# Kernel tuning notes

Measured on AMD Instinct MI355X. Metric: run time of the kernel, lower is better.

The kernel has to match this reference:

```python
import jax, jax.numpy as jnp
import numpy as np

B, L, D, K = 16, 1024, 1024, 3
EPS_LN = 1e-5    # nn.LayerNorm default eps inside SRUCell
EPS_RMS = 1e-6   # RMSNorm eps
HIGHWAY_BIAS = -2.0


def setup_inputs() -> dict:
    key = jax.random.key(0)
    ks = jax.random.split(key, 8)
    x = jax.random.normal(ks[0], (B, L, D), jnp.float32)
    conv_w = jax.random.normal(ks[1], (D, D, K), jnp.float32) * (1.0 / np.sqrt(D * K))
    conv_b = jax.random.normal(ks[2], (D,), jnp.float32) * 0.01
    ln_g = jnp.ones((D,), jnp.float32)
    ln_b = jnp.zeros((D,), jnp.float32)
    sru_w = jax.random.normal(ks[3], (D, 3 * D), jnp.float32) * (1.0 / np.sqrt(D))
    sru_v = jax.random.uniform(ks[4], (2 * D,), jnp.float32, -0.18, 0.18)
    # SRU init: forget-gate bias 0, reset-gate bias = highway_bias
    sru_b = jnp.concatenate([jnp.zeros((D,), jnp.float32),
                             jnp.full((D,), HIGHWAY_BIAS, jnp.float32)])
    lambda_w = jax.random.normal(ks[5], (D,), jnp.float32)
    rms_w = jnp.ones((D,), jnp.float32)
    return {"x": x, "conv_w": conv_w, "conv_b": conv_b, "ln_g": ln_g,
            "ln_b": ln_b, "sru_w": sru_w, "sru_v": sru_v, "sru_b": sru_b,
            "lambda_w": lambda_w, "rms_w": rms_w}


def reference(x, conv_w, conv_b, ln_g, ln_b, sru_w, sru_v, sru_b, lambda_w, rms_w):
    # --- causal conv1d: left-pad K-1 zeros, 'VALID' conv -> same length ---
    xT = jnp.transpose(x, (0, 2, 1))                      # (B, D, L)
    xp = jnp.pad(xT, ((0, 0), (0, 0), (K - 1, 0)))
    y = jax.lax.conv_general_dilated(
        xp, conv_w, window_strides=(1,), padding='VALID',
        dimension_numbers=('NCH', 'OIH', 'NCH')) + conv_b[None, :, None]
    cnn_out = jnp.transpose(y, (2, 0, 1))                 # (L, B, D) time-major

    # --- SRUCell with layer_norm=True: LN on input, then U = x @ W (k=3) ---
    mu = jnp.mean(cnn_out, -1, keepdims=True)
    var = jnp.mean((cnn_out - mu) ** 2, -1, keepdims=True)
    normed = (cnn_out - mu) * jax.lax.rsqrt(var + EPS_LN) * ln_g + ln_b
    U = jnp.einsum('lbd,de->lbe', normed, sru_w).reshape(L, B, D, 3)

    v_f, v_r = sru_v[:D], sru_v[D:]
    b_f, b_r = sru_b[:D], sru_b[D:]

    def step(c, inputs):
        u, xt = inputs                                    # u: (B, D, 3), xt: (B, D)
        u0, u1, u2 = u[..., 0], u[..., 1], u[..., 2]
        f = jax.nn.sigmoid(u1 + v_f * c + b_f)
        c_new = f * c + (1.0 - f) * u0
        r = jax.nn.sigmoid(u2 + v_r * c + b_r)
        h = r * jnp.tanh(c_new) + (1.0 - r) * xt          # highway (scale_x = 1)
        return c_new, h

    c0 = jnp.zeros((B, D), jnp.float32)
    _, h = jax.lax.scan(step, c0, (U, normed))            # h: (L, B, D)

    # --- lambda-weighted residual mix ---
    out = lambda_w * cnn_out + (1.0 - lambda_w) * h       # (L, B, D)
    out = jnp.transpose(out, (1, 0, 2))                   # (B, L, D)

    # --- RMSNorm (dropout is identity in eval) ---
    rms = out * jax.lax.rsqrt(jnp.mean(out * out, -1, keepdims=True) + EPS_RMS)
    return rms_w * rms
```

## Files before the change

### kernel.cpp

```cpp
#include <hip/hip_runtime.h>
#include <cstdint>
#include <cstddef>

#define LL 1024
#define DD 1024
#define BB 16

typedef _Float16 f16;
typedef _Float16 f16x8 __attribute__((ext_vector_type(8)));
typedef _Float16 f16x4 __attribute__((ext_vector_type(4)));
typedef float f32x4 __attribute__((ext_vector_type(4)));

__global__ __launch_bounds__(256) void xsplit_kernel(const float* __restrict__ x,
                                                     f16* __restrict__ xh) {
    int i = blockIdx.x * 256 + threadIdx.x;
    const int total = BB * LL * DD / 4;
    if (i >= total) return;
    float4 v = ((const float4*)x)[i];
    f16x4 h;
    h[0] = (f16)v.x; h[1] = (f16)v.y; h[2] = (f16)v.z; h[3] = (f16)v.w;
    ((f16x4*)xh)[i] = h;
}

__global__ __launch_bounds__(256) void wkt_kernel(const float* __restrict__ w,
                                                  f16* __restrict__ wkT) {
    int idx = blockIdx.x * 256 + threadIdx.x;
    if (idx >= 3 * DD * DD) return;
    int o = idx / 3072;
    int r = idx - o * 3072;
    int k = r >> 10, i = r & 1023;
    wkT[idx] = (f16)w[(size_t)o * 3072 + i * 3 + k];
}

__global__ __launch_bounds__(256) void swt_kernel(const float* __restrict__ w,
                                                  f16* __restrict__ swT) {
    int idx = blockIdx.x * 256 + threadIdx.x;
    if (idx >= 3 * DD * DD) return;
    int e = idx >> 10, d = idx & 1023;
    swT[idx] = (f16)w[(size_t)d * 3072 + e];
}

__global__ __launch_bounds__(256) void hgemm_kernel(
    const f16* __restrict__ A, const f16* __restrict__ BT,
    const float* __restrict__ bias, float* __restrict__ C,
    int N, int Kdim, int mode, int l0, int tpb, int Lc) {
    __shared__ f16 Asm[128 * 64];
    __shared__ f16 Bsm[128 * 64];
    const int tid = threadIdx.x;
    const int lane = tid & 63, wave = tid >> 6;
    const int wm = wave & 1, wn = wave >> 1;
    const int n0 = blockIdx.x * 128;

    int arowbase, crowbase;
    if (mode == 0) {
        arowbase = blockIdx.y * 128;
        crowbase = arowbase;
    } else {
        int bb = blockIdx.y / tpb, lt = blockIdx.y - bb * tpb;
        arowbase = (bb << 10) + l0 + lt * 128;
        crowbase = bb * Lc + lt * 128;
    }

    const int srow = tid >> 1;
    const int scb = (tid & 1) * 4;

    auto loadA = [&](int kt, f16x8 (&pa)[4]) {
#pragma unroll
        for (int q = 0; q < 4; ++q) {
            int sc = scb + q;
            if (mode == 0) {
                int m = arowbase + srow;
                int bb2 = m >> 10, l = m & 1023;
                int kc = kt >> 10;
                int t = l + kc - 2;
                int i0 = (kt & 1023) + sc * 8;
                if (t < 0) {
                    f16x8 z;
#pragma unroll
                    for (int e = 0; e < 8; ++e) z[e] = (f16)0;
                    pa[q] = z;
                } else {
                    pa[q] = *(const f16x8*)(A + (((size_t)(bb2 << 10) + t) << 10) + i0);
                }
            } else {
                pa[q] = *(const f16x8*)(A + ((size_t)(arowbase + srow) << 10) + kt + sc * 8);
            }
        }
    };
    auto loadB = [&](int kt, f16x8 (&pb)[4]) {
#pragma unroll
        for (int q = 0; q < 4; ++q) {
            int sc = scb + q;
            pb[q] = *(const f16x8*)(BT + (size_t)(n0 + srow) * Kdim + kt + sc * 8);
        }
    };
    auto store_sm = [&](f16* sm, f16x8 (&p)[4]) {
#pragma unroll
        for (int q = 0; q < 4; ++q) {
            int sc = scb + q;
            int byte = srow * 128 + ((sc * 16) ^ ((srow & 7) << 4));
            *(f16x8*)((char*)sm + byte) = p[q];
        }
    };

    f32x4 acc[4][4];
#pragma unroll
    for (int i = 0; i < 4; ++i)
#pragma unroll
        for (int j = 0; j < 4; ++j)
#pragma unroll
            for (int r = 0; r < 4; ++r) acc[i][j][r] = 0.f;

    f16x8 pa[4], pb[4];
    loadA(0, pa);
    loadB(0, pb);

    const int kbyte = (lane >> 4) * 16;
    const int rA = wm * 64 + (lane & 15);
    const int rB = wn * 64 + (lane & 15);

    for (int kt = 0; kt < Kdim; kt += 64) {
        store_sm(Asm, pa);
        store_sm(Bsm, pb);
        __syncthreads();
        if (kt + 64 < Kdim) {
            loadA(kt + 64, pa);
            loadB(kt + 64, pb);
        }
#pragma unroll
        for (int ks = 0; ks < 2; ++ks) {
            f16x8 a[4], b[4];
#pragma unroll
            for (int f = 0; f < 4; ++f) {
                int rowa = rA + f * 16;
                a[f] = *(const f16x8*)((const char*)Asm + rowa * 128 +
                                       ((ks * 64 + kbyte) ^ ((rowa & 7) << 4)));
                int rowb = rB + f * 16;
                b[f] = *(const f16x8*)((const char*)Bsm + rowb * 128 +
                                       ((ks * 64 + kbyte) ^ ((rowb & 7) << 4)));
            }
#pragma unroll
            for (int fi = 0; fi < 4; ++fi)
#pragma unroll
                for (int fj = 0; fj < 4; ++fj)
                    acc[fi][fj] = __builtin_amdgcn_mfma_f32_16x16x32_f16(
                        a[fi], b[fj], acc[fi][fj], 0, 0, 0);
        }
        __syncthreads();
    }

    float bv[4];
#pragma unroll
    for (int fj = 0; fj < 4; ++fj)
        bv[fj] = bias ? bias[n0 + wn * 64 + fj * 16 + (lane & 15)] : 0.f;
#pragma unroll
    for (int fi = 0; fi < 4; ++fi) {
        int row0 = crowbase + wm * 64 + fi * 16 + ((lane >> 4) << 2);
#pragma unroll
        for (int fj = 0; fj < 4; ++fj) {
            int col = n0 + wn * 64 + fj * 16 + (lane & 15);
            float* cp = C + (size_t)row0 * N + col;
#pragma unroll
            for (int r = 0; r < 4; ++r)
                cp[(size_t)r * N] = acc[fi][fj][r] + bv[fj];
        }
    }
}

__global__ __launch_bounds__(256) void ln_kernel(const float* __restrict__ in,
                                                 const float* __restrict__ g,
                                                 const float* __restrict__ be,
                                                 float* __restrict__ outp,
                                                 f16* __restrict__ outh) {
    const int m = blockIdx.x;
    const int t = threadIdx.x;
    const float4 v = ((const float4*)(in + ((size_t)m << 10)))[t];
    float s = v.x + v.y + v.z + v.w;
    float q = v.x * v.x + v.y * v.y + v.z * v.z + v.w * v.w;
#pragma unroll
    for (int off = 32; off; off >>= 1) {
        s += __shfl_down(s, off);
        q += __shfl_down(q, off);
    }
    __shared__ float red[8];
    const int wv = t >> 6, ln = t & 63;
    if (ln == 0) { red[wv] = s; red[4 + wv] = q; }
    __syncthreads();
    float S = red[0] + red[1] + red[2] + red[3];
    float Q = red[4] + red[5] + red[6] + red[7];
    float mu  = S * (1.f / 1024.f);
    float var = Q * (1.f / 1024.f) - mu * mu;
    float inv = rsqrtf(var + 1e-5f);
    float4 g4  = ((const float4*)g)[t];
    float4 b4  = ((const float4*)be)[t];
    float4 o;
    o.x = (v.x - mu) * inv * g4.x + b4.x;
    o.y = (v.y - mu) * inv * g4.y + b4.y;
    o.z = (v.z - mu) * inv * g4.z + b4.z;
    o.w = (v.w - mu) * inv * g4.w + b4.w;
    ((float4*)(outp + ((size_t)m << 10)))[t] = o;
    f16x4 h;
    h[0] = (f16)o.x; h[1] = (f16)o.y; h[2] = (f16)o.z; h[3] = (f16)o.w;
    ((f16x4*)(outh + ((size_t)m << 10)))[t] = h;
}

__device__ __forceinline__ float sigmoid_f(float x) {
    return __builtin_amdgcn_rcpf(1.f + __expf(-x));
}
__device__ __forceinline__ float tanh_f(float x) {
    float e = __expf(2.f * x);
    return 1.f - 2.f * __builtin_amdgcn_rcpf(e + 1.f);
}

__global__ __launch_bounds__(64) void scan_kernel(const float* __restrict__ U,
                                                  const float* __restrict__ nrm,
                                                  const float* __restrict__ cnn,
                                                  const float* __restrict__ v_in,
                                                  const float* __restrict__ b_in,
                                                  const float* __restrict__ lam,
                                                  float* __restrict__ outp,
                                                  float* __restrict__ c_state,
                                                  int l0, int Lc) {
    const int tid = blockIdx.x * 64 + threadIdx.x;
    const int b = tid >> 10, d = tid & 1023;
    const float vf = v_in[d], vr = v_in[DD + d];
    const float bf = b_in[d], br = b_in[DD + d];
    const float lw = lam[d];
    const float* Up = U + (size_t)b * Lc * 3072 + 3 * d;
    const size_t rowbase = (((size_t)(b << 10) + l0) << 10) + d;
    const float* xp = nrm + rowbase;
    const float* cp = cnn + rowbase;
    float*       op = outp + rowbase;

    float c = (l0 == 0) ? 0.f : c_state[tid];
    constexpr int CH = 8;
    float A0[CH], A1[CH], A2[CH], AX[CH], AC[CH];
    float B0[CH], B1[CH], B2[CH], BX[CH], BC[CH];

#pragma unroll
    for (int j = 0; j < CH; ++j) {
        size_t lu = (size_t)j * 3072, lx = (size_t)j << 10;
        A0[j] = Up[lu]; A1[j] = Up[lu + 1]; A2[j] = Up[lu + 2];
        AX[j] = xp[lx]; AC[j] = cp[lx];
    }

    for (int ll0 = 0; ll0 < Lc; ll0 += 2 * CH) {
#pragma unroll
        for (int j = 0; j < CH; ++j) {
            int ll = ll0 + CH + j;
            size_t lu = (size_t)ll * 3072, lx = (size_t)ll << 10;
            B0[j] = Up[lu]; B1[j] = Up[lu + 1]; B2[j] = Up[lu + 2];
            BX[j] = xp[lx]; BC[j] = cp[lx];
        }
#pragma unroll
        for (int j = 0; j < CH; ++j) {
            float f = sigmoid_f(A1[j] + vf * c + bf);
            float r = sigmoid_f(A2[j] + vr * c + br);
            float cn = fmaf(f, c - A0[j], A0[j]);
            float h  = r * tanh_f(cn) + (1.f - r) * AX[j];
            c = cn;
            op[(size_t)(ll0 + j) << 10] = fmaf(lw, AC[j] - h, h);
        }
        if (ll0 + 2 * CH < Lc) {
#pragma unroll
            for (int j = 0; j < CH; ++j) {
                int ll = ll0 + 2 * CH + j;
                size_t lu = (size_t)ll * 3072, lx = (size_t)ll << 10;
                A0[j] = Up[lu]; A1[j] = Up[lu + 1]; A2[j] = Up[lu + 2];
                AX[j] = xp[lx]; AC[j] = cp[lx];
            }
        }
#pragma unroll
        for (int j = 0; j < CH; ++j) {
            float f = sigmoid_f(B1[j] + vf * c + bf);
            float r = sigmoid_f(B2[j] + vr * c + br);
            float cn = fmaf(f, c - B0[j], B0[j]);
            float h  = r * tanh_f(cn) + (1.f - r) * BX[j];
            c = cn;
            op[(size_t)(ll0 + CH + j) << 10] = fmaf(lw, BC[j] - h, h);
        }
    }
    c_state[tid] = c;
}

__global__ __launch_bounds__(256) void rms_kernel(float* __restrict__ io,
                                                  const float* __restrict__ w) {
    const int m = blockIdx.x;
    const int t = threadIdx.x;
    float4 v = ((float4*)(io + ((size_t)m << 10)))[t];
    float q = v.x * v.x + v.y * v.y + v.z * v.z + v.w * v.w;
#pragma unroll
    for (int off = 32; off; off >>= 1) q += __shfl_down(q, off);
    __shared__ float red[4];
    const int wv = t >> 6, ln = t & 63;
    if (ln == 0) red[wv] = q;
    __syncthreads();
    float Q = red[0] + red[1] + red[2] + red[3];
    float inv = rsqrtf(Q * (1.f / 1024.f) + 1e-6f);
    float4 w4 = ((const float4*)w)[t];
    v.x *= inv * w4.x;
    v.y *= inv * w4.y;
    v.z *= inv * w4.z;
    v.w *= inv * w4.w;
    ((float4*)(io + ((size_t)m << 10)))[t] = v;
}

extern "C" void kernel_launch(void* const* d_in, const int* in_sizes, int n_in,
                              void* d_out, int out_size, void* d_ws, size_t ws_size,
                              hipStream_t stream) {
    const float* x        = (const float*)d_in[0];
    const float* conv_w   = (const float*)d_in[1];
    const float* conv_b   = (const float*)d_in[2];
    const float* ln_g     = (const float*)d_in[3];
    const float* ln_b     = (const float*)d_in[4];
    const float* sru_w    = (const float*)d_in[5];
    const float* sru_v    = (const float*)d_in[6];
    const float* sru_b    = (const float*)d_in[7];
    const float* lambda_w = (const float*)d_in[8];
    const float* rms_w    = (const float*)d_in[9];
    float* out = (float*)d_out;

    f16* x_h   = (f16*)d_ws;
    f16* nrm_h = x_h   + (size_t)16 * 1024 * 1024;
    f16* wkT   = nrm_h + (size_t)16 * 1024 * 1024;
    f16* swT   = wkT   + (size_t)3 * 1024 * 1024;
    float* cnn     = (float*)(swT + (size_t)3 * 1024 * 1024);
    float* c_state = cnn + (size_t)16 * 1024 * 1024;
    float* U_buf   = c_state + 16384;

    const size_t fixed_bytes = (size_t)38 * 1024 * 1024 * 2
                             + ((size_t)16 * 1024 * 1024 + 16384) * 4;
    int Lc = 128;
    for (int cand = 1024; cand >= 128; cand >>= 1) {
        if (fixed_bytes + (size_t)16 * cand * 3072 * 4 <= ws_size) { Lc = cand; break; }
    }
    const int tpb = Lc / 128;
    float* nrm = out;

    xsplit_kernel<<<dim3(16384), dim3(256), 0, stream>>>(x, x_h);
    wkt_kernel<<<dim3(12288), dim3(256), 0, stream>>>(conv_w, wkT);
    swt_kernel<<<dim3(12288), dim3(256), 0, stream>>>(sru_w, swT);
    hgemm_kernel<<<dim3(8, 128), dim3(256), 0, stream>>>(x_h, wkT, conv_b, cnn,
                                                         1024, 3072, 0, 0, 0, 0);
    ln_kernel<<<dim3(16384), dim3(256), 0, stream>>>(cnn, ln_g, ln_b, nrm, nrm_h);
    for (int l0 = 0; l0 < LL; l0 += Lc) {
        hgemm_kernel<<<dim3(24, 16 * tpb), dim3(256), 0, stream>>>(
            nrm_h, swT, nullptr, U_buf, 3072, 1024, 1, l0, tpb, Lc);
        scan_kernel<<<dim3(256), dim3(64), 0, stream>>>(
            U_buf, nrm, cnn, sru_v, sru_b, lambda_w, out, c_state, l0, Lc);
    }
    rms_kernel<<<dim3(16384), dim3(256), 0, stream>>>(out, rms_w);
}
```

Measured before the change: 640.5 us.

## Stage GEMM tiles directly into LDS with double-buffered async global loads

Replaces the register-staged global->LDS copy in the fp16 MFMA GEMM with global_load_lds direct-to-LDS loads into a double-buffered shared-memory tile. The next k-tile is prefetched into the alternate buffer while MFMAs run on the current one, which removes the VGPR round trip and the separate LDS store phase. Causal padding rows now read from a small zeroed buffer in global memory instead of synthesising zeros in registers. LDS use doubles to 64KB per block, which may lower occupancy, and the swizzle now moves to the global address side.

```diff
diff --git a/kernel.cpp b/kernel.cpp
--- a/kernel.cpp
+++ b/kernel.cpp
@@ -40,12 +40,16 @@
     swT[idx] = (f16)w[(size_t)d * 3072 + e];
 }
 
+__global__ __launch_bounds__(128) void zp_kernel(f16* __restrict__ zp) {
+    zp[threadIdx.x] = (f16)0;
+}
+
 __global__ __launch_bounds__(256) void hgemm_kernel(
     const f16* __restrict__ A, const f16* __restrict__ BT,
     const float* __restrict__ bias, float* __restrict__ C,
+    const f16* __restrict__ zp,
     int N, int Kdim, int mode, int l0, int tpb, int Lc) {
-    __shared__ f16 Asm[128 * 64];
-    __shared__ f16 Bsm[128 * 64];
+    __shared__ f16 sm[2][2][128 * 64];
     const int tid = threadIdx.x;
     const int lane = tid & 63, wave = tid >> 6;
     const int wm = wave & 1, wn = wave >> 1;
@@ -61,47 +65,41 @@
         crowbase = bb * Lc + lt * 128;
     }
 
-    const int srow = tid >> 1;
-    const int scb = (tid & 1) * 4;
-
-    auto loadA = [&](int kt, f16x8 (&pa)[4]) {
-#pragma unroll
-        for (int q = 0; q < 4; ++q) {
-            int sc = scb + q;
+    auto stageA = [&](int kt, int buf) {
+#pragma unroll
+        for (int i = 0; i < 4; ++i) {
+            int row = wave * 32 + i * 8 + (lane >> 3);
+            int chunk = (lane & 7) ^ (row & 7);
+            const f16* src;
             if (mode == 0) {
-                int m = arowbase + srow;
+                int m = arowbase + row;
                 int bb2 = m >> 10, l = m & 1023;
                 int kc = kt >> 10;
                 int t = l + kc - 2;
-                int i0 = (kt & 1023) + sc * 8;
-                if (t < 0) {
-                    f16x8 z;
-#pragma unroll
-                    for (int e = 0; e < 8; ++e) z[e] = (f16)0;
-                    pa[q] = z;
-                } else {
-                    pa[q] = *(const f16x8*)(A + (((size_t)(bb2 << 10) + t) << 10) + i0);
-                }
+                src = (t < 0) ? (zp + chunk * 8)
+                              : (A + (((size_t)(bb2 << 10) + t) << 10) +
+                                 (kt & 1023) + chunk * 8);
             } else {
-                pa[q] = *(const f16x8*)(A + ((size_t)(arowbase + srow) << 10) + kt + sc * 8);
+                src = A + ((size_t)(arowbase + row) << 10) + kt + chunk * 8;
             }
+            __builtin_amdgcn_global_load_lds(
+                (const __attribute__((address_space(1))) void*)src,
+                (__attribute__((address_space(3))) void*)&sm[buf][0][(wave * 32 + i * 8) * 64],
+                16, 0, 0);
         }
     };
-    auto loadB = [&](int kt, f16x8 (&pb)[4]) {
-#pragma unroll
-        for (int q = 0; q < 4; ++q) {
-            int sc = scb + q;
-            pb[q] = *(const f16x8*)(BT + (size_t)(n0 + srow) * Kdim + kt + sc * 8);
+    auto stageB = [&](int kt, int buf) {
+#pragma unroll
+        for (int i = 0; i < 4; ++i) {
+            int row = wave * 32 + i * 8 + (lane >> 3);
+            int chunk = (lane & 7) ^ (row & 7);
+            const f16* src = BT + (size_t)(n0 + row) * Kdim + kt + chunk * 8;
+            __builtin_amdgcn_global_load_lds(
+                (const __attribute__((address_space(1))) void*)src,
+                (__attribute__((address_space(3))) void*)&sm[buf][1][(wave * 32 + i * 8) * 64],
+                16, 0, 0);
         }
     };
-    auto store_sm = [&](f16* sm, f16x8 (&p)[4]) {
-#pragma unroll
-        for (int q = 0; q < 4; ++q) {
-            int sc = scb + q;
-            int byte = srow * 128 + ((sc * 16) ^ ((srow & 7) << 4));
-            *(f16x8*)((char*)sm + byte) = p[q];
-        }
-    };
 
     f32x4 acc[4][4];
 #pragma unroll
@@ -111,32 +109,33 @@
 #pragma unroll
             for (int r = 0; r < 4; ++r) acc[i][j][r] = 0.f;
 
-    f16x8 pa[4], pb[4];
-    loadA(0, pa);
-    loadB(0, pb);
+    stageA(0, 0);
+    stageB(0, 0);
+    asm volatile("s_waitcnt vmcnt(0)" ::: "memory");
+    __syncthreads();
 
     const int kbyte = (lane >> 4) * 16;
     const int rA = wm * 64 + (lane & 15);
     const int rB = wn * 64 + (lane & 15);
 
+    int cur = 0;
     for (int kt = 0; kt < Kdim; kt += 64) {
-        store_sm(Asm, pa);
-        store_sm(Bsm, pb);
-        __syncthreads();
         if (kt + 64 < Kdim) {
-            loadA(kt + 64, pa);
-            loadB(kt + 64, pb);
-        }
+            stageA(kt + 64, cur ^ 1);
+            stageB(kt + 64, cur ^ 1);
+        }
+        const char* Ap = (const char*)&sm[cur][0][0];
+        const char* Bp = (const char*)&sm[cur][1][0];
 #pragma unroll
         for (int ks = 0; ks < 2; ++ks) {
             f16x8 a[4], b[4];
 #pragma unroll
             for (int f = 0; f < 4; ++f) {
                 int rowa = rA + f * 16;
-                a[f] = *(const f16x8*)((const char*)Asm + rowa * 128 +
+                a[f] = *(const f16x8*)(Ap + rowa * 128 +
                                        ((ks * 64 + kbyte) ^ ((rowa & 7) << 4)));
                 int rowb = rB + f * 16;
-                b[f] = *(const f16x8*)((const char*)Bsm + rowb * 128 +
+                b[f] = *(const f16x8*)(Bp + rowb * 128 +
                                        ((ks * 64 + kbyte) ^ ((rowb & 7) << 4)));
             }
 #pragma unroll
@@ -146,7 +145,9 @@
                     acc[fi][fj] = __builtin_amdgcn_mfma_f32_16x16x32_f16(
                         a[fi], b[fj], acc[fi][fj], 0, 0, 0);
         }
+        asm volatile("s_waitcnt vmcnt(0)" ::: "memory");
         __syncthreads();
+        cur ^= 1;
     }
 
     float bv[4];
@@ -324,11 +325,12 @@
     f16* nrm_h = x_h   + (size_t)16 * 1024 * 1024;
     f16* wkT   = nrm_h + (size_t)16 * 1024 * 1024;
     f16* swT   = wkT   + (size_t)3 * 1024 * 1024;
-    float* cnn     = (float*)(swT + (size_t)3 * 1024 * 1024);
+    f16* zp    = swT   + (size_t)3 * 1024 * 1024;
+    float* cnn     = (float*)(zp + 1024);
     float* c_state = cnn + (size_t)16 * 1024 * 1024;
     float* U_buf   = c_state + 16384;
 
-    const size_t fixed_bytes = (size_t)38 * 1024 * 1024 * 2
+    const size_t fixed_bytes = ((size_t)38 * 1024 * 1024 + 1024) * 2
                              + ((size_t)16 * 1024 * 1024 + 16384) * 4;
     int Lc = 128;
     for (int cand = 1024; cand >= 128; cand >>= 1) {
@@ -340,12 +342,13 @@
     xsplit_kernel<<<dim3(16384), dim3(256), 0, stream>>>(x, x_h);
     wkt_kernel<<<dim3(12288), dim3(256), 0, stream>>>(conv_w, wkT);
     swt_kernel<<<dim3(12288), dim3(256), 0, stream>>>(sru_w, swT);
+    zp_kernel<<<dim3(1), dim3(128), 0, stream>>>(zp);
     hgemm_kernel<<<dim3(8, 128), dim3(256), 0, stream>>>(x_h, wkT, conv_b, cnn,
-                                                         1024, 3072, 0, 0, 0, 0);
+                                                         zp, 1024, 3072, 0, 0, 0, 0);
     ln_kernel<<<dim3(16384), dim3(256), 0, stream>>>(cnn, ln_g, ln_b, nrm, nrm_h);
     for (int l0 = 0; l0 < LL; l0 += Lc) {
         hgemm_kernel<<<dim3(24, 16 * tpb), dim3(256), 0, stream>>>(
-            nrm_h, swT, nullptr, U_buf, 3072, 1024, 1, l0, tpb, Lc);
+            nrm_h, swT, nullptr, U_buf, zp, 3072, 1024, 1, l0, tpb, Lc);
         scan_kernel<<<dim3(256), dim3(64), 0, stream>>>(
             U_buf, nrm, cnn, sru_v, sru_b, lambda_w, out, c_state, l0, Lc);
     }
```

After: 599.6 us. 1.07x faster.
